# Performance work log

Measured on AMD Instinct MI355X. Metric: run time of the kernel, lower is better.

Reference implementation:

```python
import jax, jax.numpy as jnp
import numpy as np

N_NODES = 10000
N_EDGES = 160000
DIM = 128
NLAYERS = 3
NBASIS = 16
NSPECIES = 100
CUTOFF = 5.0


def _mlp(x, W1, b1, W2, b2):
    # FullyConnectedNet([hidden, out]) with silu on hidden, linear output
    return jax.nn.silu(x @ W1 + b1) @ W2 + b2


def setup_inputs() -> dict:
    key = jax.random.key(0)
    ks = iter(jax.random.split(key, 64))
    scale = 0.08

    def w(shape):
        return jax.random.normal(next(ks), shape, dtype=jnp.float32) * scale

    inp = {
        "species": jax.random.randint(next(ks), (N_NODES,), 0, NSPECIES, dtype=jnp.int32),
        "edge_src": jnp.sort(jax.random.randint(next(ks), (N_EDGES,), 0, N_NODES, dtype=jnp.int32)),
        "edge_dst": jax.random.randint(next(ks), (N_EDGES,), 0, N_NODES, dtype=jnp.int32),
        "distances": 0.5 + 4.4 * jax.random.uniform(next(ks), (N_EDGES,), dtype=jnp.float32),
        "vec": jax.random.normal(next(ks), (N_EDGES, 3), dtype=jnp.float32),
        "switch": jax.random.uniform(next(ks), (N_EDGES,), dtype=jnp.float32),
        "species_W": w((NSPECIES, DIM)),
        "species_b": w((DIM,)),
        "radial_W": w((NLAYERS, NBASIS, DIM)),
        "radial_b": w((NLAYERS, DIM)),
    }
    for nm, out in [("a", DIM), ("F", 1), ("f", DIM), ("R", DIM), ("r", DIM), ("u", DIM)]:
        inp[nm + "_W1"] = w((NLAYERS, DIM, DIM))
        inp[nm + "_b1"] = w((NLAYERS, DIM))
        inp[nm + "_W2"] = w((NLAYERS, DIM, out))
        inp[nm + "_b2"] = w((NLAYERS, out))
    return inp


def reference(species, edge_src, edge_dst, distances, vec, switch,
              species_W, species_b, radial_W, radial_b,
              a_W1, a_b1, a_W2, a_b2,
              F_W1, F_b1, F_W2, F_b2,
              f_W1, f_b1, f_W2, f_b2,
              R_W1, R_b1, R_W2, R_b2,
              r_W1, r_b1, r_W2, r_b2,
              u_W1, u_b1, u_W2, u_b2):
    N = species.shape[0]
    # species encoding -> species_linear Dense
    xi = jax.nn.one_hot(species, NSPECIES, dtype=jnp.float32) @ species_W + species_b  # (N, dim)
    sw = switch[:, None]                                   # (E, 1)
    dirij = vec / distances[:, None] * sw                  # (E, 3)
    # gaussian radial basis on [0, cutoff]
    centers = jnp.linspace(0.0, CUTOFF, NBASIS, dtype=jnp.float32)
    eta = jnp.float32((NBASIS / CUTOFF) ** 2)
    rb = jnp.exp(-eta * (distances[:, None] - centers) ** 2)  # (E, nbasis)

    fi = None
    di = None
    for l in range(NLAYERS):
        ai = _mlp(xi, a_W1[l], a_b1[l], a_W2[l], a_b2[l])          # (N, dim)
        Dij = rb @ radial_W[l] + radial_b[l]                        # (E, dim)
        mij = ai[edge_src] * ai[edge_dst] * Dij * sw                # (E, dim)
        xi = xi + jax.ops.segment_sum(mij, edge_src, N)
        Fij = _mlp(mij, F_W1[l], F_b1[l], F_W2[l], F_b2[l]) * dirij  # (E, 3)
        fij = _mlp(mij, f_W1[l], f_b1[l], f_W2[l], f_b2[l])[:, :, None] * Fij[:, None, :]  # (E, C, 3)
        fij_sum = jax.ops.segment_sum(fij, edge_src, N)             # (N, C, 3)
        fi = fij_sum if l == 0 else fi + fij_sum
        deltai = _mlp(xi, R_W1[l], R_b1[l], R_W2[l], R_b2[l])[:, :, None] * fi  # (N, C, 3)
        if l == 0:
            di = deltai
        else:
            phi_rij = _mlp(mij, r_W1[l], r_b1[l], r_W2[l], r_b2[l])  # (E, C)
            phi_r = jax.ops.segment_sum(phi_rij * sw, edge_src, N)   # (N, C)
            di = phi_r[:, :, None] * di + deltai
        scal = jnp.sum(fi * di, axis=-1)                             # (N, C)
        dui = -_mlp(xi, u_W1[l], u_b1[l], u_W2[l], u_b2[l]) * scal   # (N, dim) since C == dim
        xi = xi + dui
    return xi
```

## Files before the change

kernel.cpp:

```cpp
#include <hip/hip_runtime.h>
#include <hip/hip_bf16.h>

#define N_NODES 10000
#define N_EDGES 160000
#define DIM     128
#define NBASIS  16
#define LDT     136

typedef __bf16 bf16x8 __attribute__((ext_vector_type(8)));
typedef __bf16 bf16x4 __attribute__((ext_vector_type(4)));
typedef __bf16 bf16x2 __attribute__((ext_vector_type(2)));
typedef float  f32x4  __attribute__((ext_vector_type(4)));

__device__ __forceinline__ float silu_f(float x){
  return x * (1.0f / (1.0f + __expf(-x)));
}
__device__ __forceinline__ f32x4 mfma16(bf16x8 a, bf16x8 b, f32x4 c){
  return __builtin_amdgcn_mfma_f32_16x16x32_bf16(a,b,c,0,0,0);
}


struct WPtrs { const float* p[11]; };

template<bool WITH_R>
__global__ __launch_bounds__(256,3) void mlp_layer(
    int nodeB,
    const __bf16* __restrict__ mij,
    const __bf16* __restrict__ fW1z, const float* __restrict__ fb1,
    const __bf16* __restrict__ fW2z, const float* __restrict__ fb2,
    const __bf16* __restrict__ FW1z, const float* __restrict__ Fb1,
    const float*  __restrict__ FW2v, const float* __restrict__ Fb2,
    const __bf16* __restrict__ rW1z, const float* __restrict__ rb1,
    const __bf16* __restrict__ rW2z, const float* __restrict__ rb2,
    const float*  __restrict__ swv,
    __bf16* __restrict__ ef, __bf16* __restrict__ ephi,
    const float* __restrict__ X,
    const __bf16* __restrict__ RW1z, const float* __restrict__ Rb1,
    const __bf16* __restrict__ RW2z, const float* __restrict__ Rb2,
    const __bf16* __restrict__ uW1z, const float* __restrict__ ub1,
    const __bf16* __restrict__ uW2z, const float* __restrict__ ub2,
    float* __restrict__ Rv, float* __restrict__ uv)
{
  __shared__ __bf16 sH[128*LDT];
  __shared__ __bf16 sW[8192];
  const int tid=threadIdx.x, lane=tid&63, wv=tid>>6, l15=lane&15, quad=lane>>4;

  if ((int)blockIdx.x < nodeB){
    const long row0n = (long)blockIdx.x*64 + wv*16;
    const long rA = row0n + l15;
    const bool okA = rA < N_NODES;

    bf16x8 fa[4];
    #pragma unroll
    for (int kc=0;kc<4;kc++){
      int kb=kc*32+quad*8;
      bf16x8 a;
      #pragma unroll
      for (int i=0;i<8;i++) a[i]=(__bf16)0.f;
      if (okA){
        float4 u0 = *(const float4*)(X + rA*DIM + kb);
        float4 u1 = *(const float4*)(X + rA*DIM + kb + 4);
        a[0]=(__bf16)u0.x;a[1]=(__bf16)u0.y;a[2]=(__bf16)u0.z;a[3]=(__bf16)u0.w;
        a[4]=(__bf16)u1.x;a[5]=(__bf16)u1.y;a[6]=(__bf16)u1.z;a[7]=(__bf16)u1.w;
      }
      fa[kc]=a;
    }

    f32x4 acc[8];
    auto zacc = [&](){
      #pragma unroll
      for (int ni=0;ni<8;++ni) acc[ni]=(f32x4){0.f,0.f,0.f,0.f};
    };
    auto gemmA = [&](const __bf16* __restrict__ Wz){
      #pragma unroll
      for (int kc=0;kc<4;kc++){
        #pragma unroll
        for (int ni=0;ni<8;ni++){
          bf16x8 w = *(const bf16x8*)(Wz + (long)(kc*512 + ni*64 + lane)*8);
          acc[ni]=mfma16(w,fa[kc],acc[ni]);
        }
      }
    };
    auto gemmH = [&](const __bf16* __restrict__ Wz){
      #pragma unroll
      for (int kc=0;kc<4;kc++){
        bf16x8 h0=*(bf16x8*)&sH[(wv*16+l15)*LDT + kc*32 + quad*8];
        #pragma unroll
        for (int ni=0;ni<8;ni++){
          bf16x8 w = *(const bf16x8*)(Wz + (long)(kc*512 + ni*64 + lane)*8);
          acc[ni]=mfma16(w,h0,acc[ni]);
        }
      }
    };
    auto hEpi = [&](const float* __restrict__ b1){
      #pragma unroll
      for (int ni=0;ni<8;++ni){
        int n0 = ni*16 + quad*4;
        float4 bb = *(const float4*)(b1 + n0);
        bf16x4 h;
        h[0]=(__bf16)silu_f(acc[ni][0]+bb.x);
        h[1]=(__bf16)silu_f(acc[ni][1]+bb.y);
        h[2]=(__bf16)silu_f(acc[ni][2]+bb.z);
        h[3]=(__bf16)silu_f(acc[ni][3]+bb.w);
        *(bf16x4*)&sH[(wv*16+l15)*LDT + n0] = h;
      }
    };
    auto cStoreF = [&](const float* __restrict__ b2, float* __restrict__ Y){
      if (okA){
        #pragma unroll
        for (int ni=0;ni<8;++ni){
          int n0 = ni*16 + quad*4;
          float4 bb = *(const float4*)(b2 + n0);
          float4 o;
          o.x=acc[ni][0]+bb.x; o.y=acc[ni][1]+bb.y;
          o.z=acc[ni][2]+bb.z; o.w=acc[ni][3]+bb.w;
          *(float4*)(Y + rA*DIM + n0) = o;
        }
      }
    };

    zacc(); gemmA(RW1z); hEpi(Rb1);
    zacc(); gemmH(RW2z); cStoreF(Rb2, Rv);
    zacc(); gemmA(uW1z); hEpi(ub1);
    zacc(); gemmH(uW2z); cStoreF(ub2, uv);
    return;
  }

  const long row0 = (long)(blockIdx.x - nodeB)*128;
  const int  rloc0 = wv*32 + l15;
  const long rB0 = row0 + rloc0, rB1 = rB0+16;

  bf16x8 fb[2][4];
  #pragma unroll
  for (int kc=0;kc<4;kc++){
    fb[0][kc] = *(const bf16x8*)(mij + rB0*DIM + kc*32 + quad*8);
    fb[1][kc] = *(const bf16x8*)(mij + rB1*DIM + kc*32 + quad*8);
  }
  float swr[2];
  if constexpr (WITH_R){ swr[0]=swv[rB0]; swr[1]=swv[rB1]; }

  f32x4 acc[2][8];
  bf16x8 pre[4];
  float eF[2];

  auto preload = [&](const __bf16* __restrict__ Wz, int half){
    #pragma unroll
    for (int it=0; it<4; ++it)
      pre[it] = *(const bf16x8*)(Wz + (long)(half*1024 + it*256 + tid)*8);
  };
  auto writePre = [&](){
    #pragma unroll
    for (int it=0; it<4; ++it)
      *(bf16x8*)&sW[(it*256+tid)*8] = pre[it];
  };
  auto zacc = [&](){
    #pragma unroll
    for (int mi=0;mi<2;++mi)
      #pragma unroll
      for (int ni=0;ni<8;++ni) acc[mi][ni]=(f32x4){0.f,0.f,0.f,0.f};
  };
  auto mfmaB = [&](int half){
    #pragma unroll
    for (int k2=0;k2<2;k2++){
      int kc = half*2 + k2;
      #pragma unroll
      for (int ni=0;ni<8;ni++){
        bf16x8 w = *(bf16x8*)&sW[(k2*512 + ni*64 + lane)*8];
        acc[0][ni]=mfma16(w,fb[0][kc],acc[0][ni]);
        acc[1][ni]=mfma16(w,fb[1][kc],acc[1][ni]);
      }
    }
  };
  auto mfmaH = [&](int half){
    #pragma unroll
    for (int k2=0;k2<2;k2++){
      int kc = half*2 + k2;
      bf16x8 h0=*(bf16x8*)&sH[(rloc0   )*LDT + kc*32 + quad*8];
      bf16x8 h1=*(bf16x8*)&sH[(rloc0+16)*LDT + kc*32 + quad*8];
      #pragma unroll
      for (int ni=0;ni<8;ni++){
        bf16x8 w = *(bf16x8*)&sW[(k2*512 + ni*64 + lane)*8];
        acc[0][ni]=mfma16(w,h0,acc[0][ni]);
        acc[1][ni]=mfma16(w,h1,acc[1][ni]);
      }
    }
  };
  auto fEpi = [&](){
    float fb2v = Fb2[0];
    #pragma unroll
    for (int mi=0;mi<2;++mi){
      float p = 0.f;
      #pragma unroll
      for (int ni=0;ni<8;++ni){
        int n0 = ni*16 + quad*4;
        float4 bb = *(const float4*)(Fb1 + n0);
        float4 w2 = *(const float4*)(FW2v + n0);
        p += silu_f(acc[mi][ni][0]+bb.x)*w2.x;
        p += silu_f(acc[mi][ni][1]+bb.y)*w2.y;
        p += silu_f(acc[mi][ni][2]+bb.z)*w2.z;
        p += silu_f(acc[mi][ni][3]+bb.w)*w2.w;
      }
      p += __shfl_xor(p,16);
      p += __shfl_xor(p,32);
      eF[mi] = p + fb2v;
    }
  };
  auto hEpi = [&](const float* __restrict__ b1){
    #pragma unroll
    for (int mi=0;mi<2;++mi){
      int rl = wv*32 + mi*16 + l15;
      #pragma unroll
      for (int ni=0;ni<8;++ni){
        int n0 = ni*16 + quad*4;
        float4 bb = *(const float4*)(b1 + n0);
        bf16x4 h;
        h[0]=(__bf16)silu_f(acc[mi][ni][0]+bb.x);
        h[1]=(__bf16)silu_f(acc[mi][ni][1]+bb.y);
        h[2]=(__bf16)silu_f(acc[mi][ni][2]+bb.z);
        h[3]=(__bf16)silu_f(acc[mi][ni][3]+bb.w);
        *(bf16x4*)&sH[rl*LDT + n0] = h;
      }
    }
  };
  auto cStore = [&](const float* __restrict__ b2, const float* mul,
                    __bf16* __restrict__ Y){
    #pragma unroll
    for (int mi=0;mi<2;++mi){
      long rg = row0 + wv*32 + mi*16 + l15;
      #pragma unroll
      for (int ni=0;ni<8;++ni){
        int n0 = ni*16 + quad*4;
        float4 bb = *(const float4*)(b2 + n0);
        bf16x4 o;
        o[0]=(__bf16)((acc[mi][ni][0]+bb.x)*mul[mi]);
        o[1]=(__bf16)((acc[mi][ni][1]+bb.y)*mul[mi]);
        o[2]=(__bf16)((acc[mi][ni][2]+bb.z)*mul[mi]);
        o[3]=(__bf16)((acc[mi][ni][3]+bb.w)*mul[mi]);
        *(bf16x4*)(Y + rg*DIM + n0) = o;
      }
    }
  };

  preload(FW1z,0);
  __syncthreads(); writePre(); __syncthreads(); preload(FW1z,1);
  zacc(); mfmaB(0);
  __syncthreads(); writePre(); __syncthreads(); preload(fW1z,0);
  mfmaB(1);
  __syncthreads(); writePre(); __syncthreads(); preload(fW1z,1);
  fEpi();
  zacc(); mfmaB(0);
  __syncthreads(); writePre(); __syncthreads(); preload(fW2z,0);
  mfmaB(1);
  __syncthreads(); writePre(); __syncthreads(); preload(fW2z,1);
  hEpi(fb1);
  zacc(); mfmaH(0);
  __syncthreads(); writePre(); __syncthreads();
  if constexpr (WITH_R) preload(rW1z,0);
  mfmaH(1);

  if constexpr (WITH_R){
    __syncthreads(); writePre(); __syncthreads(); preload(rW1z,1);
    cStore(fb2, eF, ef);
    zacc(); mfmaB(0);
    __syncthreads(); writePre(); __syncthreads(); preload(rW2z,0);
    mfmaB(1);
    __syncthreads(); writePre(); __syncthreads(); preload(rW2z,1);
    hEpi(rb1);
    zacc(); mfmaH(0);
    __syncthreads(); writePre(); __syncthreads();
    mfmaH(1);
    cStore(rb2, swr, ephi);
  } else {
    cStore(fb2, eF, ef);
  }
}

__global__ __launch_bounds__(64,4) void mlp_a(
    const float* __restrict__ X,
    const __bf16* __restrict__ W1z, const float* __restrict__ b1,
    const __bf16* __restrict__ W2z, const float* __restrict__ b2,
    __bf16* __restrict__ Y)
{
  __shared__ __bf16 sH[16*LDT];
  const int lane=threadIdx.x, l15=lane&15, quad=lane>>4;
  const long row0=(long)blockIdx.x*16;
  const long rA=row0+l15;

  bf16x8 fa[4];
  #pragma unroll
  for (int kc=0;kc<4;kc++){
    int kb=kc*32+quad*8;
    float4 u0 = *(const float4*)(X + rA*DIM + kb);
    float4 u1 = *(const float4*)(X + rA*DIM + kb + 4);
    bf16x8 a;
    a[0]=(__bf16)u0.x;a[1]=(__bf16)u0.y;a[2]=(__bf16)u0.z;a[3]=(__bf16)u0.w;
    a[4]=(__bf16)u1.x;a[5]=(__bf16)u1.y;a[6]=(__bf16)u1.z;a[7]=(__bf16)u1.w;
    fa[kc]=a;
  }

  f32x4 acc[8];
  #pragma unroll
  for (int ni=0;ni<8;++ni) acc[ni]=(f32x4){0.f,0.f,0.f,0.f};
  #pragma unroll
  for (int kc=0;kc<4;kc++){
    #pragma unroll
    for (int ni=0;ni<8;ni++){
      bf16x8 w = *(const bf16x8*)(W1z + (long)(kc*512 + ni*64 + lane)*8);
      acc[ni]=mfma16(w,fa[kc],acc[ni]);
    }
  }
  #pragma unroll
  for (int ni=0;ni<8;++ni){
    int n0 = ni*16 + quad*4;
    float4 bb = *(const float4*)(b1 + n0);
    bf16x4 h;
    h[0]=(__bf16)silu_f(acc[ni][0]+bb.x);
    h[1]=(__bf16)silu_f(acc[ni][1]+bb.y);
    h[2]=(__bf16)silu_f(acc[ni][2]+bb.z);
    h[3]=(__bf16)silu_f(acc[ni][3]+bb.w);
    *(bf16x4*)&sH[l15*LDT + n0] = h;
  }
  #pragma unroll
  for (int ni=0;ni<8;++ni) acc[ni]=(f32x4){0.f,0.f,0.f,0.f};
  #pragma unroll
  for (int kc=0;kc<4;kc++){
    bf16x8 h0=*(bf16x8*)&sH[l15*LDT + kc*32 + quad*8];
    #pragma unroll
    for (int ni=0;ni<8;ni++){
      bf16x8 w = *(const bf16x8*)(W2z + (long)(kc*512 + ni*64 + lane)*8);
      acc[ni]=mfma16(w,h0,acc[ni]);
    }
  }
  #pragma unroll
  for (int ni=0;ni<8;++ni){
    int n0 = ni*16 + quad*4;
    float4 bb = *(const float4*)(b2 + n0);
    bf16x4 o;
    o[0]=(__bf16)(acc[ni][0]+bb.x);
    o[1]=(__bf16)(acc[ni][1]+bb.y);
    o[2]=(__bf16)(acc[ni][2]+bb.z);
    o[3]=(__bf16)(acc[ni][3]+bb.w);
    *(bf16x4*)(Y + rA*DIM + n0) = o;
  }
}

__global__ __launch_bounds__(256) void setup_all(
    WPtrs wp, __bf16* __restrict__ wt,
    const int* __restrict__ esrc, int* __restrict__ row_start,
    const int* __restrict__ species, const float* __restrict__ spW,
    const float* __restrict__ spB, float* __restrict__ xi, float* __restrict__ fi,
    const float* __restrict__ dist, const float* __restrict__ vec,
    const float* __restrict__ swv, float* __restrict__ dir, float* __restrict__ rb)
{
  const int b = blockIdx.x, tid = threadIdx.x;
  if (b < 33){
    int t = b/3, l = b%3;
    const float* src = wp.p[t] + (size_t)l*16384;
    __bf16* out = wt + (size_t)b*16384;
    for (int it=0; it<8; ++it){
      int fi_ = it*256 + tid;
      int kc = fi_>>9, ni = (fi_>>6)&7, lane = fi_&63;
      int n  = ni*16 + (lane&15);
      int k0 = kc*32 + (lane>>4)*8;
      bf16x8 v;
      #pragma unroll
      for (int j=0;j<8;++j) v[j] = (__bf16)src[(k0+j)*DIM + n];
      *(bf16x8*)(out + (size_t)fi_*8) = v;
    }
  } else if (b < 73){
    int t = (b-33)*256 + tid;
    if (t <= N_NODES){
      int lo = 0, hi = N_EDGES;
      while (lo < hi){ int mid = (lo+hi)>>1; if (esrc[mid] < t) lo = mid+1; else hi = mid; }
      row_start[t] = lo;
    }
  } else if (b < 73 + 5000){
    int idx = (b-73)*256 + tid;
    int n = idx >> 7, d = idx & 127;
    xi[idx] = spW[species[n]*DIM + d] + spB[d];
    fi[n*384 + d*3 + 0] = 0.f;
    fi[n*384 + d*3 + 1] = 0.f;
    fi[n*384 + d*3 + 2] = 0.f;
  } else {
    int e = (b-5073)*256 + tid;
    if (e < N_EDGES){
      float d = dist[e];
      float s = swv[e];
      float inv = s / d;
      dir[e*3+0] = vec[e*3+0]*inv;
      dir[e*3+1] = vec[e*3+1]*inv;
      dir[e*3+2] = vec[e*3+2]*inv;
      const float eta = (16.0f/5.0f)*(16.0f/5.0f);
      #pragma unroll
      for (int j=0;j<NBASIS;j++){
        float c = (float)j * (5.0f/15.0f);
        float t2 = d - c;
        rb[e*NBASIS + j] = __expf(-eta*t2*t2);
      }
    }
  }
}

__global__ __launch_bounds__(256) void mij_segsum(
    const __bf16* __restrict__ ai, const int* __restrict__ esrc, const int* __restrict__ edst,
    const float* __restrict__ swv, const float* __restrict__ rb,
    const float* __restrict__ radW, const float* __restrict__ radB,
    __bf16* __restrict__ mij, float* __restrict__ xi)
{
  __shared__ float sRb[64*NBASIS];
  __shared__ int   sS[64], sD[64];
  __shared__ float sSw[64];
  int tid = threadIdx.x;
  int e0 = blockIdx.x * 64;
  *(float4*)(sRb + tid*4) = *(const float4*)(rb + (long)e0*NBASIS + tid*4);
  if (tid < 64){
    sS[tid]  = esrc[e0+tid];
    sD[tid]  = edst[e0+tid];
    sSw[tid] = swv[e0+tid];
  }
  const int wv = tid>>6, lane = tid&63;
  const int d = lane*2;
  float2 rw[NBASIS];
  #pragma unroll
  for (int j=0;j<NBASIS;j++)
    rw[j] = *(const float2*)(radW + j*DIM + d);
  float2 rB = *(const float2*)(radB + d);
  __syncthreads();

  float sx=0.f, sy=0.f;
  int cur = sS[wv*16];
  #pragma unroll
  for (int i=0;i<16;i++){
    int el = wv*16 + i;
    int n = sS[el];
    if (n != cur){
      atomicAdd(&xi[(long)cur*DIM+d  ], sx);
      atomicAdd(&xi[(long)cur*DIM+d+1], sy);
      sx=0.f; sy=0.f; cur=n;
    }
    bf16x2 as = *(const bf16x2*)(ai + (long)n*DIM + d);
    bf16x2 ad = *(const bf16x2*)(ai + (long)sD[el]*DIM + d);
    float acc0 = 0.f, acc1 = 0.f;
    #pragma unroll
    for (int j=0;j<NBASIS;j++){
      float rbv = sRb[el*NBASIS+j];
      acc0 += rbv*rw[j].x;
      acc1 += rbv*rw[j].y;
    }
    float sw_ = sSw[el];
    float m0 = (float)as[0]*(float)ad[0]*(acc0+rB.x)*sw_;
    float m1 = (float)as[1]*(float)ad[1]*(acc1+rB.y)*sw_;
    bf16x2 m; m[0]=(__bf16)m0; m[1]=(__bf16)m1;
    *(bf16x2*)(mij + (long)(e0+el)*DIM + d) = m;
    sx += m0; sy += m1;
  }
  atomicAdd(&xi[(long)cur*DIM+d  ], sx);
  atomicAdd(&xi[(long)cur*DIM+d+1], sy);
}

__global__ __launch_bounds__(64) void node_update(
    const __bf16* __restrict__ ef, const __bf16* __restrict__ ephi,
    const float* __restrict__ dir, const int* __restrict__ row_start,
    const float* __restrict__ Rv, const float* __restrict__ uv,
    float* __restrict__ fi, float* __restrict__ di, float* __restrict__ xi,
    float* __restrict__ out, int layer)
{
  int n = blockIdx.x, d0 = threadIdx.x*2;
  int s0 = row_start[n], s1 = row_start[n+1];
  float a[2][3] = {{0.f,0.f,0.f},{0.f,0.f,0.f}};
  float phi[2] = {0.f,0.f};
  for (int e=s0;e<s1;e++){
    bf16x2 v = *(const bf16x2*)(ef + (long)e*DIM + d0);
    float d0v = dir[e*3+0], d1v = dir[e*3+1], d2v = dir[e*3+2];
    float vx = (float)v[0], vy = (float)v[1];
    a[0][0] += vx*d0v; a[0][1] += vx*d1v; a[0][2] += vx*d2v;
    a[1][0] += vy*d0v; a[1][1] += vy*d1v; a[1][2] += vy*d2v;
    if (layer > 0){
      bf16x2 p = *(const bf16x2*)(ephi + (long)e*DIM + d0);
      phi[0] += (float)p[0]; phi[1] += (float)p[1];
    }
  }
  #pragma unroll
  for (int c=0;c<2;c++){
    int d = d0+c;
    float f0 = fi[n*384+d*3+0]+a[c][0];
    float f1 = fi[n*384+d*3+1]+a[c][1];
    float f2 = fi[n*384+d*3+2]+a[c][2];
    fi[n*384+d*3+0]=f0; fi[n*384+d*3+1]=f1; fi[n*384+d*3+2]=f2;
    float Rv_ = Rv[n*DIM+d];
    float sc = 0.f;
    float fv[3] = {f0,f1,f2};
    #pragma unroll
    for (int k=0;k<3;k++){
      float delta = Rv_*fv[k];
      float dv = (layer==0) ? delta : phi[c]*di[n*384+d*3+k] + delta;
      di[n*384+d*3+k] = dv;
      sc += fv[k]*dv;
    }
    float nx = xi[n*DIM+d] - uv[n*DIM+d]*sc;
    xi[n*DIM+d] = nx;
    if (layer == 2) out[n*DIM+d] = nx;
  }
}

extern "C" void kernel_launch(void* const* d_in, const int* in_sizes, int n_in,
                              void* d_out, int out_size, void* d_ws, size_t ws_size,
                              hipStream_t stream) {
  const int*   species = (const int*)  d_in[0];
  const int*   esrc    = (const int*)  d_in[1];
  const int*   edst    = (const int*)  d_in[2];
  const float* dist    = (const float*)d_in[3];
  const float* vec     = (const float*)d_in[4];
  const float* swv     = (const float*)d_in[5];
  const float* spW     = (const float*)d_in[6];
  const float* spB     = (const float*)d_in[7];
  const float* radW    = (const float*)d_in[8];
  const float* radB    = (const float*)d_in[9];
  const float* aW1=(const float*)d_in[10], *aB1=(const float*)d_in[11], *aW2=(const float*)d_in[12], *aB2=(const float*)d_in[13];
  const float* FW1=(const float*)d_in[14], *FB1=(const float*)d_in[15], *FW2=(const float*)d_in[16], *FB2=(const float*)d_in[17];
  const float* fW1=(const float*)d_in[18], *fB1=(const float*)d_in[19], *fW2=(const float*)d_in[20], *fB2=(const float*)d_in[21];
  const float* RW1=(const float*)d_in[22], *RB1=(const float*)d_in[23], *RW2=(const float*)d_in[24], *RB2=(const float*)d_in[25];
  const float* rW1=(const float*)d_in[26], *rB1=(const float*)d_in[27], *rW2=(const float*)d_in[28], *rB2=(const float*)d_in[29];
  const float* uW1=(const float*)d_in[30], *uB1=(const float*)d_in[31], *uW2=(const float*)d_in[32], *uB2=(const float*)d_in[33];

  const long NF = (long)N_NODES*DIM;
  const long EF = (long)N_EDGES*DIM;
  float* ws   = (float*)d_ws;
  float* xi   = ws;
  float* Rv   = xi   + NF;
  float* uv   = Rv   + NF;
  float* scal = uv   + NF;
  float* fi   = scal + NF;
  float* di   = fi   + 3*NF;
  float* dir  = di   + 3*NF;
  float* rb   = dir  + 3L*N_EDGES;
  int* row_start = (int*)(rb + 16L*N_EDGES);
  char* bp = (char*)(row_start + N_NODES + 2);
  size_t off = ((size_t)(bp - (char*)d_ws) + 15) & ~(size_t)15;
  __bf16* ai   = (__bf16*)((char*)d_ws + off);
  __bf16* mij  = ai  + NF;
  __bf16* ef   = mij + EF;
  __bf16* ephi = ef  + EF;
  __bf16* wt   = ephi + EF;

  WPtrs wp;
  wp.p[0]=aW1; wp.p[1]=aW2; wp.p[2]=FW1; wp.p[3]=fW1; wp.p[4]=fW2;
  wp.p[5]=RW1; wp.p[6]=RW2; wp.p[7]=rW1; wp.p[8]=rW2; wp.p[9]=uW1; wp.p[10]=uW2;

  setup_all<<<5698, 256, 0, stream>>>(wp, wt, esrc, row_start,
                                      species, spW, spB, xi, fi,
                                      dist, vec, swv, dir, rb);

  const int nodeB = (N_NODES + 63)/64;
  const int edgeB = N_EDGES/128;
  #define WT(t,l) (wt + (size_t)((t)*3+(l))*16384)

  for (int l=0;l<3;l++){
    const long bo = (long)l*DIM;

    mlp_a<<<N_NODES/16, 64, 0, stream>>>(xi, WT(0,l), aB1+bo, WT(1,l), aB2+bo, ai);
    mij_segsum<<<N_EDGES/64, 256, 0, stream>>>(ai, esrc, edst, swv, rb,
                                               radW + (long)l*NBASIS*DIM, radB + bo,
                                               mij, xi);
    if (l == 0)
      mlp_layer<false><<<nodeB+edgeB, 256, 0, stream>>>(
          nodeB, mij, WT(3,l), fB1+bo, WT(4,l), fB2+bo,
          WT(2,l), FB1+bo, FW2+(long)l*DIM, FB2+l,
          nullptr, nullptr, nullptr, nullptr, nullptr, ef, nullptr,
          xi, WT(5,l), RB1+bo, WT(6,l), RB2+bo,
          WT(9,l), uB1+bo, WT(10,l), uB2+bo, Rv, uv);
    else
      mlp_layer<true><<<nodeB+edgeB, 256, 0, stream>>>(
          nodeB, mij, WT(3,l), fB1+bo, WT(4,l), fB2+bo,
          WT(2,l), FB1+bo, FW2+(long)l*DIM, FB2+l,
          WT(7,l), rB1+bo, WT(8,l), rB2+bo, swv, ef, ephi,
          xi, WT(5,l), RB1+bo, WT(6,l), RB2+bo,
          WT(9,l), uB1+bo, WT(10,l), uB2+bo, Rv, uv);
    node_update<<<N_NODES, 64, 0, stream>>>(ef, ephi, dir, row_start, Rv, uv,
                                            fi, di, xi, (float*)d_out, l);
  }
}
```

Before: 545.8 us.

## Fuse edge segment reductions into MLP kernel epilogue with atomics

The edge MLP kernel no longer writes per-edge f and phi outputs as bf16 arrays to global memory. It stages them in LDS and reduces runs of equal source nodes (the edges are sorted by source) straight into the fi and phi node buffers with atomicAdd. node_update becomes a simple elementwise kernel that reads the accumulated values and resets phi for the next layer. This removes a large write-then-read round trip of edge features, in exchange for atomic traffic at block boundaries, extra LDS syncs, and float summation order that is no longer deterministic.

```diff
diff --git a/kernel.cpp b/kernel.cpp
--- a/kernel.cpp
+++ b/kernel.cpp
@@ -26,6 +26,7 @@
 __global__ __launch_bounds__(256,3) void mlp_layer(
     int nodeB,
     const __bf16* __restrict__ mij,
+    const int*    __restrict__ esrc, const float* __restrict__ dirv,
     const __bf16* __restrict__ fW1z, const float* __restrict__ fb1,
     const __bf16* __restrict__ fW2z, const float* __restrict__ fb2,
     const __bf16* __restrict__ FW1z, const float* __restrict__ Fb1,
@@ -33,7 +34,7 @@
     const __bf16* __restrict__ rW1z, const float* __restrict__ rb1,
     const __bf16* __restrict__ rW2z, const float* __restrict__ rb2,
     const float*  __restrict__ swv,
-    __bf16* __restrict__ ef, __bf16* __restrict__ ephi,
+    float* __restrict__ fiG, float* __restrict__ phiG,
     const float* __restrict__ X,
     const __bf16* __restrict__ RW1z, const float* __restrict__ Rb1,
     const __bf16* __restrict__ RW2z, const float* __restrict__ Rb2,
@@ -43,6 +44,8 @@
 {
   __shared__ __bf16 sH[128*LDT];
   __shared__ __bf16 sW[8192];
+  __shared__ int    sE[128];
+  __shared__ float  sDir[128*3];
   const int tid=threadIdx.x, lane=tid&63, wv=tid>>6, l15=lane&15, quad=lane>>4;
 
   if ((int)blockIdx.x < nodeB){
@@ -130,6 +133,10 @@
   const int  rloc0 = wv*32 + l15;
   const long rB0 = row0 + rloc0, rB1 = rB0+16;
 
+  if (tid < 32)  *(int4*)&sE[tid*4]    = *(const int4*)(esrc + row0 + tid*4);
+  if (tid >= 64 && tid < 160)
+    *(float4*)&sDir[(tid-64)*4] = *(const float4*)(dirv + row0*3 + (tid-64)*4);
+
   bf16x8 fb[2][4];
   #pragma unroll
   for (int kc=0;kc<4;kc++){
@@ -222,11 +229,10 @@
       }
     }
   };
-  auto cStore = [&](const float* __restrict__ b2, const float* mul,
-                    __bf16* __restrict__ Y){
+  auto outLDS = [&](const float* __restrict__ b2, const float* mul){
     #pragma unroll
     for (int mi=0;mi<2;++mi){
-      long rg = row0 + wv*32 + mi*16 + l15;
+      int rl = wv*32 + mi*16 + l15;
       #pragma unroll
       for (int ni=0;ni<8;++ni){
         int n0 = ni*16 + quad*4;
@@ -236,9 +242,56 @@
         o[1]=(__bf16)((acc[mi][ni][1]+bb.y)*mul[mi]);
         o[2]=(__bf16)((acc[mi][ni][2]+bb.z)*mul[mi]);
         o[3]=(__bf16)((acc[mi][ni][3]+bb.w)*mul[mi]);
-        *(bf16x4*)(Y + rg*DIM + n0) = o;
-      }
-    }
+        *(bf16x4*)&sH[rl*LDT + n0] = o;
+      }
+    }
+  };
+  auto reduceFi = [&](){
+    const int d = lane*2;
+    float a0=0.f,a1=0.f,a2=0.f,a3=0.f,a4=0.f,a5=0.f;
+    int cur = sE[wv*32];
+    for (int i=0;i<32;i++){
+      int e = wv*32+i;
+      int n = sE[e];
+      if (n != cur){
+        atomicAdd(&fiG[(long)cur*384 + d*3+0], a0);
+        atomicAdd(&fiG[(long)cur*384 + d*3+1], a1);
+        atomicAdd(&fiG[(long)cur*384 + d*3+2], a2);
+        atomicAdd(&fiG[(long)cur*384 + (d+1)*3+0], a3);
+        atomicAdd(&fiG[(long)cur*384 + (d+1)*3+1], a4);
+        atomicAdd(&fiG[(long)cur*384 + (d+1)*3+2], a5);
+        a0=a1=a2=a3=a4=a5=0.f; cur=n;
+      }
+      bf16x2 v = *(bf16x2*)&sH[e*LDT + d];
+      float vx=(float)v[0], vy=(float)v[1];
+      float d0=sDir[e*3+0], d1=sDir[e*3+1], d2=sDir[e*3+2];
+      a0+=vx*d0; a1+=vx*d1; a2+=vx*d2;
+      a3+=vy*d0; a4+=vy*d1; a5+=vy*d2;
+    }
+    atomicAdd(&fiG[(long)cur*384 + d*3+0], a0);
+    atomicAdd(&fiG[(long)cur*384 + d*3+1], a1);
+    atomicAdd(&fiG[(long)cur*384 + d*3+2], a2);
+    atomicAdd(&fiG[(long)cur*384 + (d+1)*3+0], a3);
+    atomicAdd(&fiG[(long)cur*384 + (d+1)*3+1], a4);
+    atomicAdd(&fiG[(long)cur*384 + (d+1)*3+2], a5);
+  };
+  auto reducePhi = [&](){
+    const int d = lane*2;
+    float a0=0.f,a1=0.f;
+    int cur = sE[wv*32];
+    for (int i=0;i<32;i++){
+      int e = wv*32+i;
+      int n = sE[e];
+      if (n != cur){
+        atomicAdd(&phiG[(long)cur*DIM + d  ], a0);
+        atomicAdd(&phiG[(long)cur*DIM + d+1], a1);
+        a0=a1=0.f; cur=n;
+      }
+      bf16x2 v = *(bf16x2*)&sH[e*LDT + d];
+      a0 += (float)v[0]; a1 += (float)v[1];
+    }
+    atomicAdd(&phiG[(long)cur*DIM + d  ], a0);
+    atomicAdd(&phiG[(long)cur*DIM + d+1], a1);
   };
 
   preload(FW1z,0);
@@ -257,10 +310,14 @@
   __syncthreads(); writePre(); __syncthreads();
   if constexpr (WITH_R) preload(rW1z,0);
   mfmaH(1);
+  outLDS(fb2, eF);
+  __syncthreads();
+  if constexpr (WITH_R) writePre();
+  reduceFi();
+  __syncthreads();
 
   if constexpr (WITH_R){
-    __syncthreads(); writePre(); __syncthreads(); preload(rW1z,1);
-    cStore(fb2, eF, ef);
+    preload(rW1z,1);
     zacc(); mfmaB(0);
     __syncthreads(); writePre(); __syncthreads(); preload(rW2z,0);
     mfmaB(1);
@@ -269,9 +326,9 @@
     zacc(); mfmaH(0);
     __syncthreads(); writePre(); __syncthreads();
     mfmaH(1);
-    cStore(rb2, swr, ephi);
-  } else {
-    cStore(fb2, eF, ef);
+    outLDS(rb2, swr);
+    __syncthreads();
+    reducePhi();
   }
 }
 
@@ -349,6 +406,7 @@
     const int* __restrict__ esrc, int* __restrict__ row_start,
     const int* __restrict__ species, const float* __restrict__ spW,
     const float* __restrict__ spB, float* __restrict__ xi, float* __restrict__ fi,
+    float* __restrict__ phi,
     const float* __restrict__ dist, const float* __restrict__ vec,
     const float* __restrict__ swv, float* __restrict__ dir, float* __restrict__ rb)
 {
@@ -378,6 +436,7 @@
     int idx = (b-73)*256 + tid;
     int n = idx >> 7, d = idx & 127;
     xi[idx] = spW[species[n]*DIM + d] + spB[d];
+    phi[idx] = 0.f;
     fi[n*384 + d*3 + 0] = 0.f;
     fi[n*384 + d*3 + 1] = 0.f;
     fi[n*384 + d*3 + 2] = 0.f;
@@ -458,49 +517,32 @@
   atomicAdd(&xi[(long)cur*DIM+d+1], sy);
 }
 
-__global__ __launch_bounds__(64) void node_update(
-    const __bf16* __restrict__ ef, const __bf16* __restrict__ ephi,
-    const float* __restrict__ dir, const int* __restrict__ row_start,
+__global__ __launch_bounds__(256) void node_update(
     const float* __restrict__ Rv, const float* __restrict__ uv,
     float* __restrict__ fi, float* __restrict__ di, float* __restrict__ xi,
-    float* __restrict__ out, int layer)
+    float* __restrict__ phi, float* __restrict__ out, int layer)
 {
-  int n = blockIdx.x, d0 = threadIdx.x*2;
-  int s0 = row_start[n], s1 = row_start[n+1];
-  float a[2][3] = {{0.f,0.f,0.f},{0.f,0.f,0.f}};
-  float phi[2] = {0.f,0.f};
-  for (int e=s0;e<s1;e++){
-    bf16x2 v = *(const bf16x2*)(ef + (long)e*DIM + d0);
-    float d0v = dir[e*3+0], d1v = dir[e*3+1], d2v = dir[e*3+2];
-    float vx = (float)v[0], vy = (float)v[1];
-    a[0][0] += vx*d0v; a[0][1] += vx*d1v; a[0][2] += vx*d2v;
-    a[1][0] += vy*d0v; a[1][1] += vy*d1v; a[1][2] += vy*d2v;
-    if (layer > 0){
-      bf16x2 p = *(const bf16x2*)(ephi + (long)e*DIM + d0);
-      phi[0] += (float)p[0]; phi[1] += (float)p[1];
-    }
-  }
-  #pragma unroll
-  for (int c=0;c<2;c++){
-    int d = d0+c;
-    float f0 = fi[n*384+d*3+0]+a[c][0];
-    float f1 = fi[n*384+d*3+1]+a[c][1];
-    float f2 = fi[n*384+d*3+2]+a[c][2];
-    fi[n*384+d*3+0]=f0; fi[n*384+d*3+1]=f1; fi[n*384+d*3+2]=f2;
-    float Rv_ = Rv[n*DIM+d];
-    float sc = 0.f;
-    float fv[3] = {f0,f1,f2};
-    #pragma unroll
-    for (int k=0;k<3;k++){
-      float delta = Rv_*fv[k];
-      float dv = (layer==0) ? delta : phi[c]*di[n*384+d*3+k] + delta;
-      di[n*384+d*3+k] = dv;
-      sc += fv[k]*dv;
-    }
-    float nx = xi[n*DIM+d] - uv[n*DIM+d]*sc;
-    xi[n*DIM+d] = nx;
-    if (layer == 2) out[n*DIM+d] = nx;
-  }
+  int idx = blockIdx.x*256 + threadIdx.x;
+  int n = idx >> 7;
+  int d = idx & 127;
+  float f0 = fi[n*384+d*3+0];
+  float f1 = fi[n*384+d*3+1];
+  float f2 = fi[n*384+d*3+2];
+  float phi_v = (layer > 0) ? phi[idx] : 0.f;
+  float Rv_ = Rv[idx];
+  float sc = 0.f;
+  float fv[3] = {f0,f1,f2};
+  #pragma unroll
+  for (int k=0;k<3;k++){
+    float delta = Rv_*fv[k];
+    float dv = (layer==0) ? delta : phi_v*di[n*384+d*3+k] + delta;
+    di[n*384+d*3+k] = dv;
+    sc += fv[k]*dv;
+  }
+  float nx = xi[idx] - uv[idx]*sc;
+  xi[idx] = nx;
+  phi[idx] = 0.f;
+  if (layer == 2) out[idx] = nx;
 }
 
 extern "C" void kernel_launch(void* const* d_in, const int* in_sizes, int n_in,
@@ -529,8 +571,8 @@
   float* xi   = ws;
   float* Rv   = xi   + NF;
   float* uv   = Rv   + NF;
-  float* scal = uv   + NF;
-  float* fi   = scal + NF;
+  float* phi  = uv   + NF;
+  float* fi   = phi  + NF;
   float* di   = fi   + 3*NF;
   float* dir  = di   + 3*NF;
   float* rb   = dir  + 3L*N_EDGES;
@@ -539,16 +581,14 @@
   size_t off = ((size_t)(bp - (char*)d_ws) + 15) & ~(size_t)15;
   __bf16* ai   = (__bf16*)((char*)d_ws + off);
   __bf16* mij  = ai  + NF;
-  __bf16* ef   = mij + EF;
-  __bf16* ephi = ef  + EF;
-  __bf16* wt   = ephi + EF;
+  __bf16* wt   = mij + EF;
 
   WPtrs wp;
   wp.p[0]=aW1; wp.p[1]=aW2; wp.p[2]=FW1; wp.p[3]=fW1; wp.p[4]=fW2;
   wp.p[5]=RW1; wp.p[6]=RW2; wp.p[7]=rW1; wp.p[8]=rW2; wp.p[9]=uW1; wp.p[10]=uW2;
 
   setup_all<<<5698, 256, 0, stream>>>(wp, wt, esrc, row_start,
-                                      species, spW, spB, xi, fi,
+                                      species, spW, spB, xi, fi, phi,
                                       dist, vec, swv, dir, rb);
 
   const int nodeB = (N_NODES + 63)/64;
@@ -564,19 +604,23 @@
                                                mij, xi);
     if (l == 0)
       mlp_layer<false><<<nodeB+edgeB, 256, 0, stream>>>(
-          nodeB, mij, WT(3,l), fB1+bo, WT(4,l), fB2+bo,
+          nodeB, mij, esrc, dir,
+          WT(3,l), fB1+bo, WT(4,l), fB2+bo,
           WT(2,l), FB1+bo, FW2+(long)l*DIM, FB2+l,
-          nullptr, nullptr, nullptr, nullptr, nullptr, ef, nullptr,
+          nullptr, nullptr, nullptr, nullptr, nullptr,
+          fi, phi,
           xi, WT(5,l), RB1+bo, WT(6,l), RB2+bo,
           WT(9,l), uB1+bo, WT(10,l), uB2+bo, Rv, uv);
     else
       mlp_layer<true><<<nodeB+edgeB, 256, 0, stream>>>(
-          nodeB, mij, WT(3,l), fB1+bo, WT(4,l), fB2+bo,
+          nodeB, mij, esrc, dir,
+          WT(3,l), fB1+bo, WT(4,l), fB2+bo,
           WT(2,l), FB1+bo, FW2+(long)l*DIM, FB2+l,
-          WT(7,l), rB1+bo, WT(8,l), rB2+bo, swv, ef, ephi,
+          WT(7,l), rB1+bo, WT(8,l), rB2+bo, swv,
+          fi, phi,
           xi, WT(5,l), RB1+bo, WT(6,l), RB2+bo,
           WT(9,l), uB1+bo, WT(10,l), uB2+bo, Rv, uv);
-    node_update<<<N_NODES, 64, 0, stream>>>(ef, ephi, dir, row_start, Rv, uv,
-                                            fi, di, xi, (float*)d_out, l);
-  }
-}
+    node_update<<<5000, 256, 0, stream>>>(Rv, uv, fi, di, xi, phi,
+                                          (float*)d_out, l);
+  }
+}
```

Result: slower. 714.9 us (+31.0%).
